# Performance work log

Hardware: AMD Instinct MI355X
Metric: run time of the kernel (lower is better)

Reference implementation:

```python
import jax, jax.numpy as jnp
import numpy as np

N = 12288
IN_F = 256
OUT_F = 128
ALPHA = 0.2  # LeakyReLU negative slope


def setup_inputs() -> dict:
    key = jax.random.key(0)
    k_x, k_adj, k_w, k_a1, k_a2 = jax.random.split(key, 5)
    x = jax.random.normal(k_x, (N, IN_F), dtype=jnp.float32)
    adj = jax.random.randint(k_adj, (N, N), 0, 2, dtype=jnp.int32)
    # Learned params (nn.Linear without bias). Kaiming-uniform-ish init scale.
    W = jax.random.normal(k_w, (IN_F, OUT_F), dtype=jnp.float32) / np.sqrt(IN_F)
    a1 = jax.random.normal(k_a1, (OUT_F,), dtype=jnp.float32) / np.sqrt(OUT_F)
    a2 = jax.random.normal(k_a2, (OUT_F,), dtype=jnp.float32) / np.sqrt(OUT_F)
    return {"x": x, "adj": adj, "W": W, "a1": a1, "a2": a2}


def reference(x, adj, W, a1, a2):
    # h = tran(x): [N, OUT_F]
    h = x @ W
    # e[i, j] = att1(h)[j] + att2(h)[i]  (unsqueeze(0) + unsqueeze(1))
    s1 = h @ a1  # [N]
    s2 = h @ a2  # [N]
    e = s1[None, :] + s2[:, None]            # [N, N]
    e = jnp.where(e > 0, e, ALPHA * e)       # LeakyReLU
    e = jnp.where(adj > 0, e, -jnp.inf)      # mask non-edges
    attn = jax.nn.softmax(e, axis=1)         # row softmax (dropout=0 / eval)
    return attn @ h                          # [N, OUT_F]
```

## Files before the change

kernel.cpp:

```cpp
#include <hip/hip_runtime.h>
#include <hip/hip_bf16.h>

constexpr int NR = 12288;
constexpr int KF = 256;
constexpr int DF = 128;
#define NEGBIG (-1e30f)

typedef __attribute__((ext_vector_type(8))) __bf16 bf16x8;
typedef __attribute__((ext_vector_type(4))) float  f32x4;

__device__ __forceinline__ unsigned short f2bf(float f) {
    union { float f; unsigned u; } v; v.f = f;
    unsigned r = v.u + 0x7FFFu + ((v.u >> 16) & 1u);
    return (unsigned short)(r >> 16);
}

__global__ __launch_bounds__(256) void k_gemm_h(
    const float* __restrict__ x, const float* __restrict__ W,
    float* __restrict__ h, unsigned short* __restrict__ hbT)
{
    __shared__ __align__(16) float xs[64][65];
    __shared__ __align__(16) float ws[64][132];
    const int t  = threadIdx.x;
    const int tx = t & 15, ty = t >> 4;
    const int rowbase = blockIdx.x * 64;

    float acc[4][8];
#pragma unroll
    for (int i = 0; i < 4; ++i)
#pragma unroll
        for (int j = 0; j < 8; ++j) acc[i][j] = 0.f;

    for (int kt = 0; kt < KF; kt += 64) {
        {
            int row = t >> 2, k0 = (t & 3) * 16;
            const float4* src = (const float4*)(x + (size_t)(rowbase + row) * KF + kt + k0);
            float4 v0 = src[0], v1 = src[1], v2 = src[2], v3 = src[3];
            xs[row][k0+ 0]=v0.x; xs[row][k0+ 1]=v0.y; xs[row][k0+ 2]=v0.z; xs[row][k0+ 3]=v0.w;
            xs[row][k0+ 4]=v1.x; xs[row][k0+ 5]=v1.y; xs[row][k0+ 6]=v1.z; xs[row][k0+ 7]=v1.w;
            xs[row][k0+ 8]=v2.x; xs[row][k0+ 9]=v2.y; xs[row][k0+10]=v2.z; xs[row][k0+11]=v2.w;
            xs[row][k0+12]=v3.x; xs[row][k0+13]=v3.y; xs[row][k0+14]=v3.z; xs[row][k0+15]=v3.w;
        }
        {
            int k = t >> 2, c0 = (t & 3) * 32;
            const float4* src = (const float4*)(W + (size_t)(kt + k) * DF + c0);
#pragma unroll
            for (int j = 0; j < 8; ++j)
                *(float4*)&ws[k][c0 + j * 4] = src[j];
        }
        __syncthreads();
#pragma unroll 4
        for (int k = 0; k < 64; ++k) {
            float xv[4];
#pragma unroll
            for (int ri = 0; ri < 4; ++ri) xv[ri] = xs[ty * 4 + ri][k];
            float4 w0 = *(float4*)&ws[k][tx * 8];
            float4 w1 = *(float4*)&ws[k][tx * 8 + 4];
#pragma unroll
            for (int ri = 0; ri < 4; ++ri) {
                acc[ri][0] += xv[ri] * w0.x; acc[ri][1] += xv[ri] * w0.y;
                acc[ri][2] += xv[ri] * w0.z; acc[ri][3] += xv[ri] * w0.w;
                acc[ri][4] += xv[ri] * w1.x; acc[ri][5] += xv[ri] * w1.y;
                acc[ri][6] += xv[ri] * w1.z; acc[ri][7] += xv[ri] * w1.w;
            }
        }
        __syncthreads();
    }
#pragma unroll
    for (int ri = 0; ri < 4; ++ri) {
        int row = rowbase + ty * 4 + ri;
        *(float4*)(h + (size_t)row * DF + tx * 8)     = make_float4(acc[ri][0], acc[ri][1], acc[ri][2], acc[ri][3]);
        *(float4*)(h + (size_t)row * DF + tx * 8 + 4) = make_float4(acc[ri][4], acc[ri][5], acc[ri][6], acc[ri][7]);
    }
#pragma unroll
    for (int ci = 0; ci < 8; ++ci) {
        int col = tx * 8 + ci;
        ushort4 u;
        u.x = f2bf(acc[0][ci]); u.y = f2bf(acc[1][ci]);
        u.z = f2bf(acc[2][ci]); u.w = f2bf(acc[3][ci]);
        *(ushort4*)(hbT + (size_t)col * NR + rowbase + ty * 4) = u;
    }
}

__global__ __launch_bounds__(256) void k_s12(
    const float* __restrict__ h, const float* __restrict__ a1,
    const float* __restrict__ a2, float* __restrict__ s1, float* __restrict__ s2)
{
    const int lane = threadIdx.x & 63;
    const int row  = blockIdx.x * 4 + (threadIdx.x >> 6);
    const float* hr = h + (size_t)row * DF;
    float h0 = hr[lane], h1 = hr[lane + 64];
    float p1 = h0 * a1[lane] + h1 * a1[lane + 64];
    float p2 = h0 * a2[lane] + h1 * a2[lane + 64];
#pragma unroll
    for (int off = 32; off > 0; off >>= 1) {
        p1 += __shfl_xor(p1, off);
        p2 += __shfl_xor(p2, off);
    }
    if (lane == 0) { s1[row] = p1; s2[row] = p2; }
}

__global__ __launch_bounds__(256) void k_flash(
    const int* __restrict__ adj, const unsigned short* __restrict__ hbT,
    const float* __restrict__ s1, const float* __restrict__ s2,
    float* __restrict__ num, float* __restrict__ mC, float* __restrict__ lC,
    int CW)
{
    __shared__ __align__(16) unsigned short hbt[128][40];
    const int t    = threadIdx.x;
    const int wid  = t >> 6, lane = t & 63;
    const int r    = lane & 15, g = lane >> 4;
    const int rowb = blockIdx.x * 64;
    const int prow = rowb + wid * 16 + r;
    const int chunk = blockIdx.y;
    const int j0base = chunk * CW;

    const float s2r = s2[prow];
    float m = NEGBIG, lpart = 0.f;
    f32x4 acc[8];
#pragma unroll
    for (int f = 0; f < 8; ++f) acc[f] = f32x4{0.f, 0.f, 0.f, 0.f};

    const int*   ap = adj + (size_t)prow * NR + j0base + g * 8;
    const float* sp = s1 + j0base + g * 8;
    const int sf = t >> 1, sc = (t & 1) * 16;
    const unsigned short* hsrc = hbT + (size_t)sf * NR + j0base + sc;

    const int nsteps = CW >> 5;
    for (int it = 0; it < nsteps; ++it) {
        bf16x8 v0 = *(const bf16x8*)(hsrc);
        bf16x8 v1 = *(const bf16x8*)(hsrc + 8);
        hsrc += 32;
        *(bf16x8*)&hbt[sf][sc]     = v0;
        *(bf16x8*)&hbt[sf][sc + 8] = v1;
        __syncthreads();

        const int4   aa = *(const int4*)(ap);
        const int4   ab = *(const int4*)(ap + 4);
        const float4 sa = *(const float4*)(sp);
        const float4 sb = *(const float4*)(sp + 4);
        ap += 32; sp += 32;

        int   msk[8] = {aa.x, aa.y, aa.z, aa.w, ab.x, ab.y, ab.z, ab.w};
        float ev[8]  = {sa.x, sa.y, sa.z, sa.w, sb.x, sb.y, sb.z, sb.w};
#pragma unroll
        for (int i = 0; i < 8; ++i) {
            float v = ev[i] + s2r;
            v = fmaxf(v, 0.2f * v);
            ev[i] = (msk[i] > 0) ? v : NEGBIG;
        }
        float tm = fmaxf(fmaxf(fmaxf(ev[0], ev[1]), fmaxf(ev[2], ev[3])),
                         fmaxf(fmaxf(ev[4], ev[5]), fmaxf(ev[6], ev[7])));
        tm = fmaxf(tm, __shfl_xor(tm, 16));
        tm = fmaxf(tm, __shfl_xor(tm, 32));
        const float mnew = fmaxf(m, tm);
        const float al   = __expf(m - mnew);
        m = mnew;

        float ps = 0.f;
        bf16x8 pfrag;
#pragma unroll
        for (int i = 0; i < 8; ++i) {
            float p = (msk[i] > 0) ? __expf(ev[i] - mnew) : 0.f;
            ps += p;
            pfrag[i] = (__bf16)p;
        }
        lpart = lpart * al + ps;

        float a4[4];
#pragma unroll
        for (int q = 0; q < 4; ++q) a4[q] = __shfl(al, (g << 2) | q);
#pragma unroll
        for (int f = 0; f < 8; ++f) {
            acc[f][0] *= a4[0]; acc[f][1] *= a4[1];
            acc[f][2] *= a4[2]; acc[f][3] *= a4[3];
        }
#pragma unroll
        for (int f = 0; f < 8; ++f) {
            bf16x8 bfrag = *(const bf16x8*)&hbt[f * 16 + r][g * 8];
            acc[f] = __builtin_amdgcn_mfma_f32_16x16x32_bf16(pfrag, bfrag, acc[f], 0, 0, 0);
        }
        __syncthreads();
    }

    lpart += __shfl_xor(lpart, 16);
    lpart += __shfl_xor(lpart, 32);
    if (g == 0) {
        mC[(size_t)chunk * NR + prow] = m;
        lC[(size_t)chunk * NR + prow] = lpart;
    }
    float* nb = num + (size_t)chunk * NR * DF;
#pragma unroll
    for (int f = 0; f < 8; ++f)
#pragma unroll
        for (int q = 0; q < 4; ++q) {
            int row = rowb + wid * 16 + g * 4 + q;
            nb[(size_t)row * DF + f * 16 + r] = acc[f][q];
        }
}

__global__ __launch_bounds__(256) void k_comb(
    const float* __restrict__ num, const float* __restrict__ mC,
    const float* __restrict__ lC, float* __restrict__ out, int CH)
{
    const int t   = threadIdx.x;
    const int row = blockIdx.x * 2 + (t >> 7);
    const int f   = t & 127;
    float M = NEGBIG;
    for (int c = 0; c < CH; ++c) M = fmaxf(M, mC[(size_t)c * NR + row]);
    float L = 0.f, o = 0.f;
    for (int c = 0; c < CH; ++c) {
        float w = __expf(mC[(size_t)c * NR + row] - M);
        L += lC[(size_t)c * NR + row] * w;
        o += num[(size_t)c * NR * DF + (size_t)row * DF + f] * w;
    }
    out[(size_t)row * DF + f] = o / L;
}

extern "C" void kernel_launch(void* const* d_in, const int* in_sizes, int n_in,
                              void* d_out, int out_size, void* d_ws, size_t ws_size,
                              hipStream_t stream)
{
    const float* x   = (const float*)d_in[0];
    const int*   adj = (const int*)d_in[1];
    const float* W   = (const float*)d_in[2];
    const float* a1  = (const float*)d_in[3];
    const float* a2  = (const float*)d_in[4];
    float* out = (float*)d_out;

    char* p = (char*)d_ws;
    float*          h   = (float*)p;          p += (size_t)NR * DF * 4;
    unsigned short* hbT = (unsigned short*)p; p += (size_t)DF * NR * 2;
    float*          s1  = (float*)p;          p += (size_t)NR * 4;
    float*          s2  = (float*)p;          p += (size_t)NR * 4;
    size_t base = (size_t)(p - (char*)d_ws);
    size_t per  = (size_t)NR * DF * 4 + 2 * (size_t)NR * 4;
    int CH = 4;
    while (CH > 1 && base + (size_t)CH * per > ws_size) CH >>= 1;
    float* numb = (float*)p; p += (size_t)CH * NR * DF * 4;
    float* mC   = (float*)p; p += (size_t)CH * NR * 4;
    float* lC   = (float*)p;

    k_gemm_h<<<NR / 64, 256, 0, stream>>>(x, W, h, hbT);
    k_s12<<<NR / 4, 256, 0, stream>>>(h, a1, a2, s1, s2);
    k_flash<<<dim3(NR / 64, CH), 256, 0, stream>>>(adj, hbT, s1, s2, numb, mC, lC, NR / CH);
    k_comb<<<NR / 2, 256, 0, stream>>>(numb, mC, lC, out, CH);
}
```

Baseline: 266.1 us.

## Use static per-row softmax bound, fuse score projection into GEMM, drop LDS staging

Computes the attention scores s1/s2 inside the projection GEMM epilogue, removing the separate kernel and the fp32 h buffer. The flash kernel now takes an upper bound on each row's max from the global max of s1 (LeakyReLU is monotone), which removes the online rescaling, the per-step max reductions and the per-chunk max outputs, so the combine step only sums. B fragments are read straight from global memory instead of through LDS with barriers, the step is widened to 64 columns with two MFMAs, and occupancy is hinted via launch bounds. Risks: every block redundantly scans s1 for the global max, and rows whose true max sits far below the bound could underflow in exp. The uncoalesced global B loads may also cost more than the LDS path did.

Result: slower. 406.4 us (+52.7%).

```diff
diff --git a/kernel.cpp b/kernel.cpp
--- a/kernel.cpp
+++ b/kernel.cpp
@@ -17,7 +17,8 @@
 
 __global__ __launch_bounds__(256) void k_gemm_h(
     const float* __restrict__ x, const float* __restrict__ W,
-    float* __restrict__ h, unsigned short* __restrict__ hbT)
+    const float* __restrict__ a1, const float* __restrict__ a2,
+    unsigned short* __restrict__ hbT, float* __restrict__ s1, float* __restrict__ s2)
 {
     __shared__ __align__(16) float xs[64][65];
     __shared__ __align__(16) float ws[64][132];
@@ -67,12 +68,6 @@
         __syncthreads();
     }
 #pragma unroll
-    for (int ri = 0; ri < 4; ++ri) {
-        int row = rowbase + ty * 4 + ri;
-        *(float4*)(h + (size_t)row * DF + tx * 8)     = make_float4(acc[ri][0], acc[ri][1], acc[ri][2], acc[ri][3]);
-        *(float4*)(h + (size_t)row * DF + tx * 8 + 4) = make_float4(acc[ri][4], acc[ri][5], acc[ri][6], acc[ri][7]);
-    }
-#pragma unroll
     for (int ci = 0; ci < 8; ++ci) {
         int col = tx * 8 + ci;
         ushort4 u;
@@ -80,115 +75,109 @@
         u.z = f2bf(acc[2][ci]); u.w = f2bf(acc[3][ci]);
         *(ushort4*)(hbT + (size_t)col * NR + rowbase + ty * 4) = u;
     }
-}
-
-__global__ __launch_bounds__(256) void k_s12(
-    const float* __restrict__ h, const float* __restrict__ a1,
-    const float* __restrict__ a2, float* __restrict__ s1, float* __restrict__ s2)
-{
-    const int lane = threadIdx.x & 63;
-    const int row  = blockIdx.x * 4 + (threadIdx.x >> 6);
-    const float* hr = h + (size_t)row * DF;
-    float h0 = hr[lane], h1 = hr[lane + 64];
-    float p1 = h0 * a1[lane] + h1 * a1[lane + 64];
-    float p2 = h0 * a2[lane] + h1 * a2[lane + 64];
-#pragma unroll
-    for (int off = 32; off > 0; off >>= 1) {
-        p1 += __shfl_xor(p1, off);
-        p2 += __shfl_xor(p2, off);
-    }
-    if (lane == 0) { s1[row] = p1; s2[row] = p2; }
-}
-
-__global__ __launch_bounds__(256) void k_flash(
+    float4 a1lo = *(const float4*)(a1 + tx * 8), a1hi = *(const float4*)(a1 + tx * 8 + 4);
+    float4 a2lo = *(const float4*)(a2 + tx * 8), a2hi = *(const float4*)(a2 + tx * 8 + 4);
+#pragma unroll
+    for (int ri = 0; ri < 4; ++ri) {
+        float p1 = acc[ri][0]*a1lo.x + acc[ri][1]*a1lo.y + acc[ri][2]*a1lo.z + acc[ri][3]*a1lo.w
+                 + acc[ri][4]*a1hi.x + acc[ri][5]*a1hi.y + acc[ri][6]*a1hi.z + acc[ri][7]*a1hi.w;
+        float p2 = acc[ri][0]*a2lo.x + acc[ri][1]*a2lo.y + acc[ri][2]*a2lo.z + acc[ri][3]*a2lo.w
+                 + acc[ri][4]*a2hi.x + acc[ri][5]*a2hi.y + acc[ri][6]*a2hi.z + acc[ri][7]*a2hi.w;
+#pragma unroll
+        for (int off = 8; off > 0; off >>= 1) {
+            p1 += __shfl_xor(p1, off);
+            p2 += __shfl_xor(p2, off);
+        }
+        if (tx == 0) {
+            s1[rowbase + ty * 4 + ri] = p1;
+            s2[rowbase + ty * 4 + ri] = p2;
+        }
+    }
+}
+
+__global__ __launch_bounds__(256, 3) void k_flash(
     const int* __restrict__ adj, const unsigned short* __restrict__ hbT,
     const float* __restrict__ s1, const float* __restrict__ s2,
-    float* __restrict__ num, float* __restrict__ mC, float* __restrict__ lC,
-    int CW)
-{
-    __shared__ __align__(16) unsigned short hbt[128][40];
+    float* __restrict__ num, float* __restrict__ lC, int CW)
+{
     const int t    = threadIdx.x;
     const int wid  = t >> 6, lane = t & 63;
     const int r    = lane & 15, g = lane >> 4;
     const int rowb = blockIdx.x * 64;
     const int prow = rowb + wid * 16 + r;
     const int chunk = blockIdx.y;
-    const int j0base = chunk * CW;
+    const int j0 = chunk * CW;
+
+    __shared__ float gred[4];
+    float gm = NEGBIG;
+    const float4* s14 = (const float4*)s1;
+    for (int i = t; i < NR / 4; i += 256) {
+        float4 v = s14[i];
+        gm = fmaxf(fmaxf(v.x, v.y), fmaxf(fmaxf(v.z, v.w), gm));
+    }
+#pragma unroll
+    for (int off = 32; off > 0; off >>= 1) gm = fmaxf(gm, __shfl_xor(gm, off));
+    if (lane == 0) gred[wid] = gm;
+    __syncthreads();
+    gm = fmaxf(fmaxf(gred[0], gred[1]), fmaxf(gred[2], gred[3]));
 
     const float s2r = s2[prow];
-    float m = NEGBIG, lpart = 0.f;
+    const float zub = s2r + gm;
+    const float Mi  = fmaxf(zub, 0.2f * zub);
+
+    float lsum = 0.f;
     f32x4 acc[8];
 #pragma unroll
     for (int f = 0; f < 8; ++f) acc[f] = f32x4{0.f, 0.f, 0.f, 0.f};
 
-    const int*   ap = adj + (size_t)prow * NR + j0base + g * 8;
-    const float* sp = s1 + j0base + g * 8;
-    const int sf = t >> 1, sc = (t & 1) * 16;
-    const unsigned short* hsrc = hbT + (size_t)sf * NR + j0base + sc;
-
-    const int nsteps = CW >> 5;
+    const int*   ap = adj + (size_t)prow * NR + j0 + g * 8;
+    const float* sp = s1 + j0 + g * 8;
+    const unsigned short* hp = hbT + (size_t)r * NR + j0 + g * 8;
+
+    const int nsteps = CW >> 6;
     for (int it = 0; it < nsteps; ++it) {
-        bf16x8 v0 = *(const bf16x8*)(hsrc);
-        bf16x8 v1 = *(const bf16x8*)(hsrc + 8);
-        hsrc += 32;
-        *(bf16x8*)&hbt[sf][sc]     = v0;
-        *(bf16x8*)&hbt[sf][sc + 8] = v1;
-        __syncthreads();
-
-        const int4   aa = *(const int4*)(ap);
-        const int4   ab = *(const int4*)(ap + 4);
-        const float4 sa = *(const float4*)(sp);
-        const float4 sb = *(const float4*)(sp + 4);
-        ap += 32; sp += 32;
-
-        int   msk[8] = {aa.x, aa.y, aa.z, aa.w, ab.x, ab.y, ab.z, ab.w};
-        float ev[8]  = {sa.x, sa.y, sa.z, sa.w, sb.x, sb.y, sb.z, sb.w};
-#pragma unroll
-        for (int i = 0; i < 8; ++i) {
-            float v = ev[i] + s2r;
-            v = fmaxf(v, 0.2f * v);
-            ev[i] = (msk[i] > 0) ? v : NEGBIG;
-        }
-        float tm = fmaxf(fmaxf(fmaxf(ev[0], ev[1]), fmaxf(ev[2], ev[3])),
-                         fmaxf(fmaxf(ev[4], ev[5]), fmaxf(ev[6], ev[7])));
-        tm = fmaxf(tm, __shfl_xor(tm, 16));
-        tm = fmaxf(tm, __shfl_xor(tm, 32));
-        const float mnew = fmaxf(m, tm);
-        const float al   = __expf(m - mnew);
-        m = mnew;
-
-        float ps = 0.f;
-        bf16x8 pfrag;
-#pragma unroll
-        for (int i = 0; i < 8; ++i) {
-            float p = (msk[i] > 0) ? __expf(ev[i] - mnew) : 0.f;
-            ps += p;
-            pfrag[i] = (__bf16)p;
-        }
-        lpart = lpart * al + ps;
-
-        float a4[4];
-#pragma unroll
-        for (int q = 0; q < 4; ++q) a4[q] = __shfl(al, (g << 2) | q);
+        const int4   aa0 = *(const int4*)(ap);
+        const int4   aa1 = *(const int4*)(ap + 4);
+        const int4   ab0 = *(const int4*)(ap + 32);
+        const int4   ab1 = *(const int4*)(ap + 36);
+        const float4 sa0 = *(const float4*)(sp);
+        const float4 sa1 = *(const float4*)(sp + 4);
+        const float4 sb0 = *(const float4*)(sp + 32);
+        const float4 sb1 = *(const float4*)(sp + 36);
+        ap += 64; sp += 64;
+
+        bf16x8 pf0, pf1;
+#define PROC(mm, ss, dst, idx) { \
+            float t0 = (ss) + s2r; \
+            float lr = fmaxf(t0, 0.2f * t0); \
+            float e  = ((mm) > 0) ? lr : NEGBIG; \
+            float p  = __expf(e - Mi); \
+            lsum += p; \
+            dst[idx] = (__bf16)p; }
+        PROC(aa0.x, sa0.x, pf0, 0) PROC(aa0.y, sa0.y, pf0, 1)
+        PROC(aa0.z, sa0.z, pf0, 2) PROC(aa0.w, sa0.w, pf0, 3)
+        PROC(aa1.x, sa1.x, pf0, 4) PROC(aa1.y, sa1.y, pf0, 5)
+        PROC(aa1.z, sa1.z, pf0, 6) PROC(aa1.w, sa1.w, pf0, 7)
+        PROC(ab0.x, sb0.x, pf1, 0) PROC(ab0.y, sb0.y, pf1, 1)
+        PROC(ab0.z, sb0.z, pf1, 2) PROC(ab0.w, sb0.w, pf1, 3)
+        PROC(ab1.x, sb1.x, pf1, 4) PROC(ab1.y, sb1.y, pf1, 5)
+        PROC(ab1.z, sb1.z, pf1, 6) PROC(ab1.w, sb1.w, pf1, 7)
+#undef PROC
+
 #pragma unroll
         for (int f = 0; f < 8; ++f) {
-            acc[f][0] *= a4[0]; acc[f][1] *= a4[1];
-            acc[f][2] *= a4[2]; acc[f][3] *= a4[3];
-        }
-#pragma unroll
-        for (int f = 0; f < 8; ++f) {
-            bf16x8 bfrag = *(const bf16x8*)&hbt[f * 16 + r][g * 8];
-            acc[f] = __builtin_amdgcn_mfma_f32_16x16x32_bf16(pfrag, bfrag, acc[f], 0, 0, 0);
-        }
-        __syncthreads();
-    }
-
-    lpart += __shfl_xor(lpart, 16);
-    lpart += __shfl_xor(lpart, 32);
-    if (g == 0) {
-        mC[(size_t)chunk * NR + prow] = m;
-        lC[(size_t)chunk * NR + prow] = lpart;
-    }
+            const unsigned short* rowp = hp + (size_t)f * (16 * NR) + (size_t)it * 64;
+            bf16x8 b0 = *(const bf16x8*)(rowp);
+            bf16x8 b1 = *(const bf16x8*)(rowp + 32);
+            acc[f] = __builtin_amdgcn_mfma_f32_16x16x32_bf16(pf0, b0, acc[f], 0, 0, 0);
+            acc[f] = __builtin_amdgcn_mfma_f32_16x16x32_bf16(pf1, b1, acc[f], 0, 0, 0);
+        }
+    }
+
+    lsum += __shfl_xor(lsum, 16);
+    lsum += __shfl_xor(lsum, 32);
+    if (g == 0) lC[(size_t)chunk * NR + prow] = lsum;
+
     float* nb = num + (size_t)chunk * NR * DF;
 #pragma unroll
     for (int f = 0; f < 8; ++f)
@@ -200,19 +189,16 @@
 }
 
 __global__ __launch_bounds__(256) void k_comb(
-    const float* __restrict__ num, const float* __restrict__ mC,
-    const float* __restrict__ lC, float* __restrict__ out, int CH)
+    const float* __restrict__ num, const float* __restrict__ lC,
+    float* __restrict__ out, int CH)
 {
     const int t   = threadIdx.x;
     const int row = blockIdx.x * 2 + (t >> 7);
     const int f   = t & 127;
-    float M = NEGBIG;
-    for (int c = 0; c < CH; ++c) M = fmaxf(M, mC[(size_t)c * NR + row]);
     float L = 0.f, o = 0.f;
     for (int c = 0; c < CH; ++c) {
-        float w = __expf(mC[(size_t)c * NR + row] - M);
-        L += lC[(size_t)c * NR + row] * w;
-        o += num[(size_t)c * NR * DF + (size_t)row * DF + f] * w;
+        L += lC[(size_t)c * NR + row];
+        o += num[(size_t)c * NR * DF + (size_t)row * DF + f];
     }
     out[(size_t)row * DF + f] = o / L;
 }
@@ -229,20 +215,17 @@
     float* out = (float*)d_out;
 
     char* p = (char*)d_ws;
-    float*          h   = (float*)p;          p += (size_t)NR * DF * 4;
     unsigned short* hbT = (unsigned short*)p; p += (size_t)DF * NR * 2;
     float*          s1  = (float*)p;          p += (size_t)NR * 4;
     float*          s2  = (float*)p;          p += (size_t)NR * 4;
     size_t base = (size_t)(p - (char*)d_ws);
-    size_t per  = (size_t)NR * DF * 4 + 2 * (size_t)NR * 4;
+    size_t per  = (size_t)NR * DF * 4 + (size_t)NR * 4;
     int CH = 4;
     while (CH > 1 && base + (size_t)CH * per > ws_size) CH >>= 1;
     float* numb = (float*)p; p += (size_t)CH * NR * DF * 4;
-    float* mC   = (float*)p; p += (size_t)CH * NR * 4;
     float* lC   = (float*)p;
 
-    k_gemm_h<<<NR / 64, 256, 0, stream>>>(x, W, h, hbT);
-    k_s12<<<NR / 4, 256, 0, stream>>>(h, a1, a2, s1, s2);
-    k_flash<<<dim3(NR / 64, CH), 256, 0, stream>>>(adj, hbT, s1, s2, numb, mC, lC, NR / CH);
-    k_comb<<<NR / 2, 256, 0, stream>>>(numb, mC, lC, out, CH);
-}
+    k_gemm_h<<<NR / 64, 256, 0, stream>>>(x, W, a1, a2, hbT, s1, s2);
+    k_flash<<<dim3(NR / 64, CH), 256, 0, stream>>>(adj, hbT, s1, s2, numb, lC, NR / CH);
+    k_comb<<<NR / 2, 256, 0, stream>>>(numb, lC, out, CH);
+}
```
